# Kernel tuning notes

Measured on AMD Instinct MI355X. Metric: run time of the kernel, lower is better.

The kernel has to match this reference:

```python
import jax, jax.numpy as jnp
import numpy as np
from jax import lax

N, D, H = 8192, 256, 128
EPS = 1e-5


def _layernorm(x, g, b):
    m = jnp.mean(x, axis=-1, keepdims=True)
    v = jnp.mean((x - m) ** 2, axis=-1, keepdims=True)
    return (x - m) * jax.lax.rsqrt(v + EPS) * g + b


def setup_inputs() -> dict:
    key = jax.random.key(0)
    ks = jax.random.split(key, 8)
    s = 1.0 / np.sqrt(D)
    return {
        "x": jax.random.normal(ks[0], (N, D), jnp.float32),
        "wq": jax.random.normal(ks[1], (D, D), jnp.float32) * s,
        "bq": jnp.zeros((D,), jnp.float32),
        "wk": jax.random.normal(ks[2], (D, D), jnp.float32) * s,
        "bk": jnp.zeros((D,), jnp.float32),
        "wv": jax.random.normal(ks[3], (D, D), jnp.float32) * s,
        "bv": jnp.zeros((D,), jnp.float32),
        "cw": jax.random.normal(ks[4], (1, 1, 3, 3), jnp.float32) / 3.0,
        "cb": jnp.zeros((1,), jnp.float32),
        "m1w": jax.random.normal(ks[5], (H, D), jnp.float32) * s,
        "m2w": jax.random.normal(ks[6], (D, H), jnp.float32) / np.sqrt(H),
        "bng": jnp.ones((H,), jnp.float32),
        "bnb": jnp.zeros((H,), jnp.float32),
        "ln1g": jnp.ones((D,), jnp.float32),
        "ln1b": jnp.zeros((D,), jnp.float32),
        "ln2g": jnp.ones((D,), jnp.float32),
        "ln2b": jnp.zeros((D,), jnp.float32),
    }


def reference(x, wq, bq, wk, bk, wv, bv, cw, cb, m1w, m2w, bng, bnb, ln1g, ln1b, ln2g, ln2b):
    q = x @ wq.T + bq            # [N, D]
    k = x @ wk.T + bk
    v = x @ wv.T + bv
    # global Frobenius-norm normalization (torch.norm(q, p=2) over whole tensor)
    q = q / jnp.linalg.norm(q)
    k = k / jnp.linalg.norm(k)
    A = q @ k.T                  # [N, N]
    # 3x3 conv2d, 1->1 channel, padding SAME
    A4 = A[None, None, :, :]
    A4 = lax.conv_general_dilated(A4, cw, window_strides=(1, 1), padding="SAME")
    A4 = A4 + cb[None, :, None, None]
    agg_A = A4[0, 0]             # [N, N]
    attn = agg_A @ v             # [N, D]
    h = x + _layernorm(attn, ln1g, ln1b)
    # MLP with BatchNorm1d (training-mode batch stats, biased var)
    z = _layernorm(h, ln2g, ln2b) @ m1w.T          # [N, H]
    mu = jnp.mean(z, axis=0)
    var = jnp.mean((z - mu) ** 2, axis=0)
    z = (z - mu) * jax.lax.rsqrt(var + EPS) * bng + bnb
    z = jax.nn.relu(z)
    out = h + z @ m2w.T
    return out
```

## Files before the change

### kernel.cpp

```cpp
#include <hip/hip_runtime.h>
#include <hip/hip_bf16.h>
#include <math.h>


#define N_ 8192
#define D_ 256
#define H_ 128
#define EPSF 1e-5f

typedef unsigned short ushort_t;
typedef unsigned int uint_t;
typedef __attribute__((ext_vector_type(8))) short bf16x8;
typedef __attribute__((ext_vector_type(4))) short bf16x4;
typedef __attribute__((ext_vector_type(4))) float f32x4;

static const size_t OFF_QB  = 0;
static const size_t OFF_KT  = 4195328;
static const size_t OFF_VT  = 8389632;
static const size_t OFF_GP  = 12588032;
static const size_t OFF_MT  = 25170944;
static const size_t OFF_SVP = 25564160;
static const size_t OFF_SVC = 25826304;
static const size_t OFF_RED = 25827328;
static const size_t OFF_ZSP = 25829376;
static const size_t OFF_BNS = 26353664;
static const size_t OFF_WC  = 26354688;
static const size_t OFF_M1C = 26747904;
static const size_t OFF_M2C = 26813440;
static const size_t OFF_XB  = 26878976;
static const size_t WS_NEED = 31073280;

__device__ __forceinline__ ushort_t f2bf(float f) {
    __hip_bfloat16 h = __float2bfloat16(f);
    return reinterpret_cast<ushort_t&>(h);
}

__device__ __forceinline__ bf16x8 cvt8(float4 f0, float4 f1) {
    bf16x8 o;
    o[0] = (short)f2bf(f0.x); o[1] = (short)f2bf(f0.y);
    o[2] = (short)f2bf(f0.z); o[3] = (short)f2bf(f0.w);
    o[4] = (short)f2bf(f1.x); o[5] = (short)f2bf(f1.y);
    o[6] = (short)f2bf(f1.z); o[7] = (short)f2bf(f1.w);
    return o;
}

__device__ __forceinline__ float waveSum(float v)
{
#pragma unroll
    for (int o = 32; o > 0; o >>= 1) v += __shfl_xor(v, o);
    return v;
}

__global__ void prep_w(const float* __restrict__ wq, const float* __restrict__ wk,
                       const float* __restrict__ wv, const float* __restrict__ m1w,
                       const float* __restrict__ m2w, const float* __restrict__ x,
                       ushort_t* __restrict__ WC, ushort_t* __restrict__ M1C,
                       ushort_t* __restrict__ M2C, ushort_t* __restrict__ XB,
                       ushort_t* __restrict__ QbG, ushort_t* __restrict__ VTC)
{
    const int bid = blockIdx.x, tid = threadIdx.x;
    if (bid < 96) {
        const int sel = bid >> 5, kb = bid & 31;
        const float* W = (sel == 0) ? wq : ((sel == 1) ? wk : wv);
        const float* p = W + (size_t)tid * 256 + kb * 8;
        *(bf16x8*)(WC + (size_t)sel * 65536 + (size_t)kb * 2048 + (size_t)tid * 8)
            = cvt8(*(const float4*)p, *(const float4*)(p + 4));
    } else if (bid < 128) {
        const int kb = bid - 96;
        if (tid < 128) {
            const float* p = m1w + (size_t)tid * 256 + kb * 8;
            *(bf16x8*)(M1C + (size_t)kb * 1024 + (size_t)tid * 8)
                = cvt8(*(const float4*)p, *(const float4*)(p + 4));
        }
    } else if (bid < 144) {
        const int kb = bid - 128;
        const float* p = m2w + (size_t)tid * 128 + kb * 8;
        *(bf16x8*)(M2C + (size_t)kb * 2048 + (size_t)tid * 8)
            = cvt8(*(const float4*)p, *(const float4*)(p + 4));
    } else if (bid == 144) {
        QbG[tid] = 0; QbG[(size_t)8193 * 256 + tid] = 0;
        VTC[(size_t)tid * 8] = 0;
        VTC[((size_t)1024 * 256 + tid) * 8 + 1] = 0;
    } else {
        const size_t lin = (size_t)(bid - 145) * 2048 + (size_t)tid * 8;
        const float* p = x + lin;
        *(bf16x8*)(XB + lin) = cvt8(*(const float4*)p, *(const float4*)(p + 4));
    }
}

__global__ void __launch_bounds__(256)
qkv_mfma(const ushort_t* __restrict__ XB, const ushort_t* __restrict__ WC,
         const float* __restrict__ bq, const float* __restrict__ bk,
         const float* __restrict__ bv,
         ushort_t* __restrict__ QbG, ushort_t* __restrict__ KTC,
         ushort_t* __restrict__ VTC,
         float* __restrict__ RED, float* __restrict__ SVP)
{
    __shared__ ushort_t XS[32][264];
    __shared__ float lds4[4];
    const int tid = threadIdx.x, lane = tid & 63, wid = tid >> 6;
    const int sel = blockIdx.y;
    const int i0 = blockIdx.x * 32;
    const int jw = wid * 64;
    const int l15 = lane & 15, kg = lane >> 4;
    const ushort_t* Wc = WC + (size_t)sel * 65536;
    const float* B = (sel == 0) ? bq : ((sel == 1) ? bk : bv);

#pragma unroll
    for (int p = 0; p < 4; ++p) {
        int lin = p * 256 + tid;
        int row = lin >> 5;
        int c8  = (lin & 31) * 8;
        *(bf16x8*)(&XS[row][c8]) = *(const bf16x8*)(XB + (size_t)(i0 + row) * 256 + c8);
    }
    __syncthreads();

    f32x4 acc[2][4];
#pragma unroll
    for (int mi = 0; mi < 2; ++mi)
#pragma unroll
        for (int ni = 0; ni < 4; ++ni) acc[mi][ni] = 0.0f;

    for (int k0 = 0; k0 < 256; k0 += 32) {
        bf16x8 a[2], b[4];
#pragma unroll
        for (int mi = 0; mi < 2; ++mi)
            a[mi] = *(const bf16x8*)(&XS[16 * mi + l15][k0 + 8 * kg]);
#pragma unroll
        for (int ni = 0; ni < 4; ++ni)
            b[ni] = *(const bf16x8*)(Wc + (size_t)((k0 >> 3) + kg) * 2048
                                        + (size_t)(jw + 16 * ni + l15) * 8);
#pragma unroll
        for (int mi = 0; mi < 2; ++mi)
#pragma unroll
            for (int ni = 0; ni < 4; ++ni)
                acc[mi][ni] = __builtin_amdgcn_mfma_f32_16x16x32_bf16(a[mi], b[ni], acc[mi][ni], 0, 0, 0);
    }

    float ssq = 0.0f;
    float colp[4] = {0.0f, 0.0f, 0.0f, 0.0f};

    if (sel == 0) {
#pragma unroll
        for (int mi = 0; mi < 2; ++mi)
#pragma unroll
            for (int ni = 0; ni < 4; ++ni) {
                const int col = jw + 16 * ni + l15;
                const float bias = B[col];
#pragma unroll
                for (int r = 0; r < 4; ++r) {
                    const int row = i0 + 16 * mi + 4 * kg + r;
                    float val = acc[mi][ni][r] + bias;
                    QbG[(size_t)(row + 1) * 256 + col] = f2bf(val);
                    ssq = fmaf(val, val, ssq);
                }
            }
    } else if (sel == 1) {
#pragma unroll
        for (int mi = 0; mi < 2; ++mi)
#pragma unroll
            for (int ni = 0; ni < 4; ++ni) {
                const int col = jw + 16 * ni + l15;
                const float bias = B[col];
                const int tb = i0 + 16 * mi + 4 * kg;
                bf16x4 pk;
#pragma unroll
                for (int r = 0; r < 4; ++r) {
                    float val = acc[mi][ni][r] + bias;
                    ssq = fmaf(val, val, ssq);
                    pk[r] = (short)f2bf(val);
                }
                *(bf16x4*)(KTC + ((size_t)(tb >> 3) * 256 + col) * 8 + (tb & 7)) = pk;
            }
    } else {
#pragma unroll
        for (int mi = 0; mi < 2; ++mi)
#pragma unroll
            for (int ni = 0; ni < 4; ++ni) {
                const int col = jw + 16 * ni + l15;
                const float bias = B[col];
                const int tb = i0 + 16 * mi + 4 * kg;
                const int cb = tb >> 3, e0 = (tb & 7) + 1;
                float v0 = acc[mi][ni][0] + bias, v1 = acc[mi][ni][1] + bias;
                float v2 = acc[mi][ni][2] + bias, v3 = acc[mi][ni][3] + bias;
                colp[ni] += v0 + v1 + v2 + v3;
                ushort_t* p = VTC + ((size_t)cb * 256 + col) * 8 + e0;
                p[0] = f2bf(v0);
                *(uint_t*)(p + 1) = (uint_t)f2bf(v1) | ((uint_t)f2bf(v2) << 16);
                ushort_t v3b = f2bf(v3);
                if (e0 == 5)
                    VTC[((size_t)(cb + 1) * 256 + col) * 8] = v3b;
                else
                    p[3] = v3b;
            }
    }

    if (sel < 2) {
        float s = ssq;
#pragma unroll
        for (int o = 32; o > 0; o >>= 1) s += __shfl_down(s, o);
        if (lane == 0) lds4[wid] = s;
        __syncthreads();
        if (tid == 0)
            RED[sel * 256 + blockIdx.x] = lds4[0] + lds4[1] + lds4[2] + lds4[3];
    } else {
#pragma unroll
        for (int ni = 0; ni < 4; ++ni) {
            float v = colp[ni];
            v += __shfl_xor(v, 16);
            v += __shfl_xor(v, 32);
            if (kg == 0)
                SVP[(size_t)blockIdx.x * 256 + jw + 16 * ni + l15] = v;
        }
    }
}

__global__ void __launch_bounds__(256)
g_mfma(const ushort_t* __restrict__ KTC, const ushort_t* __restrict__ VTC,
       float* __restrict__ GP)
{
    const int tid = threadIdx.x, lane = tid & 63, wid = tid >> 6;
    const int d0 = blockIdx.x * 64 + (wid >> 1) * 32;
    const int jw = blockIdx.y * 32 + (wid & 1) * 16;
    const int ks = blockIdx.z;
    const int l15 = lane & 15, kg = lane >> 4;

    f32x4 acc[3][2];
#pragma unroll
    for (int v = 0; v < 3; ++v) { acc[v][0] = 0.0f; acc[v][1] = 0.0f; }

    for (int tt = 0; tt < 512; tt += 32) {
        const int t0 = ks * 512 + tt;
        const int cb0 = (t0 >> 3) + kg;
        bf16x8 a[2];
#pragma unroll
        for (int mi = 0; mi < 2; ++mi)
            a[mi] = *(const bf16x8*)(KTC + ((size_t)cb0 * 256 + (d0 + 16 * mi + l15)) * 8);

        const int j = jw + l15;
        uint4 r0 = *(const uint4*)(VTC + ((size_t)cb0 * 256 + j) * 8);
        uint_t rx = *(const uint_t*)(VTC + ((size_t)(cb0 + 1) * 256 + j) * 8);
        uint4 r2;
        r2.x = r0.y; r2.y = r0.z; r2.z = r0.w; r2.w = rx;
        uint4 m1;
        m1.x = (r0.x >> 16) | (r2.x << 16);
        m1.y = (r0.y >> 16) | (r2.y << 16);
        m1.z = (r0.z >> 16) | (r2.z << 16);
        m1.w = (r0.w >> 16) | (r2.w << 16);
        bf16x8 b2 = __builtin_bit_cast(bf16x8, r0);
        bf16x8 b0 = __builtin_bit_cast(bf16x8, r2);
        bf16x8 b1 = __builtin_bit_cast(bf16x8, m1);
#pragma unroll
        for (int mi = 0; mi < 2; ++mi) {
            acc[0][mi] = __builtin_amdgcn_mfma_f32_16x16x32_bf16(a[mi], b0, acc[0][mi], 0, 0, 0);
            acc[1][mi] = __builtin_amdgcn_mfma_f32_16x16x32_bf16(a[mi], b1, acc[1][mi], 0, 0, 0);
            acc[2][mi] = __builtin_amdgcn_mfma_f32_16x16x32_bf16(a[mi], b2, acc[2][mi], 0, 0, 0);
        }
    }

#pragma unroll
    for (int v = 0; v < 3; ++v) {
        float* gp = GP + (size_t)(ks * 3 + v) * 65536;
#pragma unroll
        for (int mi = 0; mi < 2; ++mi)
#pragma unroll
            for (int r = 0; r < 4; ++r)
                gp[(size_t)(d0 + 16 * mi + 4 * kg + r) * 256 + (jw + l15)]
                    = acc[v][mi][r];
    }
}

__global__ void combine_m(const float* __restrict__ GP, const float* __restrict__ cw,
                          const float* __restrict__ RED, const float* __restrict__ SVP,
                          const float* __restrict__ cb,
                          ushort_t* __restrict__ MTc, float* __restrict__ SVC)
{
    __shared__ float lds8[8];
    __shared__ float scsh;
    const int d = blockIdx.x, j = threadIdx.x;

    float sq = RED[j], sk = RED[256 + j];
#pragma unroll
    for (int o = 32; o > 0; o >>= 1) { sq += __shfl_down(sq, o); sk += __shfl_down(sk, o); }
    if ((j & 63) == 0) { lds8[j >> 6] = sq; lds8[4 + (j >> 6)] = sk; }

    float g[3] = {0.0f, 0.0f, 0.0f};
    for (int ks = 0; ks < 16; ++ks)
#pragma unroll
        for (int v = 0; v < 3; ++v)
            g[v] += GP[(size_t)(ks * 3 + v) * 65536 + (size_t)d * 256 + j];

    __syncthreads();
    if (j == 0) {
        float SQ = lds8[0] + lds8[1] + lds8[2] + lds8[3];
        float SK = lds8[4] + lds8[5] + lds8[6] + lds8[7];
        scsh = rsqrtf(SQ) * rsqrtf(SK);
    }
    __syncthreads();
    const float sc = scsh;

#pragma unroll
    for (int u = 0; u < 3; ++u) {
        float m = sc * (cw[u * 3 + 0] * g[0] + cw[u * 3 + 1] * g[1] + cw[u * 3 + 2] * g[2]);
        MTc[(size_t)u * 65536 + (size_t)(d >> 3) * 2048 + (size_t)j * 8 + (d & 7)]
            = f2bf(m);
    }
    if (d == 0) {
        float s = 0.0f;
        for (int b = 0; b < 256; ++b) s += SVP[(size_t)b * 256 + j];
        SVC[j] = cb[0] * s;
    }
}

__global__ void __launch_bounds__(512)
attn_ln_z_mfma(const ushort_t* __restrict__ QbG, const ushort_t* __restrict__ MTc,
               const float* __restrict__ SVC, const float* __restrict__ x,
               const float* __restrict__ ln1g, const float* __restrict__ ln1b,
               const float* __restrict__ ln2g, const float* __restrict__ ln2b,
               const ushort_t* __restrict__ M1C,
               float* __restrict__ h, float* __restrict__ Z,
               float* __restrict__ ZSP)
{
    __shared__ ushort_t QS[18][264];
    __shared__ float OUT[16][260];
    const int tid = threadIdx.x, lane = tid & 63, wid = tid >> 6;
    const int i0 = blockIdx.x * 16;
    const int jw = wid * 32;
    const int l15 = lane & 15, kg = lane >> 4;

    float4 xpre0 = *(const float4*)(x + (size_t)(i0 + wid * 2 + 0) * 256 + lane * 4);
    float4 xpre1 = *(const float4*)(x + (size_t)(i0 + wid * 2 + 1) * 256 + lane * 4);

    {
        int row = tid >> 5, c8 = (tid & 31) * 8;
        *(bf16x8*)(&QS[row][c8]) = *(const bf16x8*)(QbG + (size_t)(i0 + row) * 256 + c8);
        int idx = tid + 512;
        if (idx < 576) {
            row = idx >> 5; c8 = (idx & 31) * 8;
            *(bf16x8*)(&QS[row][c8]) = *(const bf16x8*)(QbG + (size_t)(i0 + row) * 256 + c8);
        }
    }
    __syncthreads();

    f32x4 acc[2];
    acc[0] = 0.0f; acc[1] = 0.0f;

    for (int k0 = 0; k0 < 256; k0 += 32) {
        bf16x8 a[3], b[3][2];
#pragma unroll
        for (int u = 0; u < 3; ++u)
            a[u] = *(const bf16x8*)(&QS[l15 + u][k0 + 8 * kg]);
#pragma unroll
        for (int u = 0; u < 3; ++u)
#pragma unroll
            for (int ni = 0; ni < 2; ++ni)
                b[u][ni] = *(const bf16x8*)(MTc + (size_t)u * 65536
                    + (size_t)((k0 >> 3) + kg) * 2048
                    + (size_t)(jw + 16 * ni + l15) * 8);
#pragma unroll
        for (int ni = 0; ni < 2; ++ni)
#pragma unroll
            for (int u = 0; u < 3; ++u)
                acc[ni] = __builtin_amdgcn_mfma_f32_16x16x32_bf16(
                    a[u], b[u][ni], acc[ni], 0, 0, 0);
    }

#pragma unroll
    for (int ni = 0; ni < 2; ++ni) {
        const int col = jw + 16 * ni + l15;
        const float sv = SVC[col];
#pragma unroll
        for (int r = 0; r < 4; ++r)
            OUT[4 * kg + r][col] = acc[ni][r] + sv;
    }
    __syncthreads();

    const float4 g14 = *(const float4*)(ln1g + lane * 4);
    const float4 b14 = *(const float4*)(ln1b + lane * 4);
    const float4 g24 = *(const float4*)(ln2g + lane * 4);
    const float4 b24 = *(const float4*)(ln2b + lane * 4);
#pragma unroll
    for (int rr = 0; rr < 2; ++rr) {
        const int row_l = wid * 2 + rr;
        const size_t off = (size_t)(i0 + row_l) * 256 + lane * 4;

        float4 a4 = *(const float4*)&OUT[row_l][lane * 4];
        float m = waveSum(a4.x + a4.y + a4.z + a4.w) * (1.0f / D_);
        float4 d4 = make_float4(a4.x - m, a4.y - m, a4.z - m, a4.w - m);
        float var = waveSum(d4.x * d4.x + d4.y * d4.y + d4.z * d4.z + d4.w * d4.w) * (1.0f / D_);
        float rs = rsqrtf(var + EPSF);

        float4 x4 = (rr == 0) ? xpre0 : xpre1;
        float4 h4;
        h4.x = x4.x + d4.x * rs * g14.x + b14.x;
        h4.y = x4.y + d4.y * rs * g14.y + b14.y;
        h4.z = x4.z + d4.z * rs * g14.z + b14.z;
        h4.w = x4.w + d4.w * rs * g14.w + b14.w;
        *(float4*)(h + off) = h4;

        float m2 = waveSum(h4.x + h4.y + h4.z + h4.w) * (1.0f / D_);
        float4 e4 = make_float4(h4.x - m2, h4.y - m2, h4.z - m2, h4.w - m2);
        float v2 = waveSum(e4.x * e4.x + e4.y * e4.y + e4.z * e4.z + e4.w * e4.w) * (1.0f / D_);
        float rs2 = rsqrtf(v2 + EPSF);

        float4 o4;
        o4.x = e4.x * rs2 * g24.x + b24.x;
        o4.y = e4.y * rs2 * g24.y + b24.y;
        o4.z = e4.z * rs2 * g24.z + b24.z;
        o4.w = e4.w * rs2 * g24.w + b24.w;
        *(float4*)&OUT[row_l][lane * 4] = o4;
    }
    __syncthreads();

    const int jz = wid * 16;
    f32x4 zacc;
    zacc = 0.0f;

    for (int k0 = 0; k0 < 256; k0 += 32) {
        bf16x8 a, b;
        {
            const float* lp = &OUT[l15][k0 + 8 * kg];
            a = cvt8(*(const float4*)lp, *(const float4*)(lp + 4));
        }
        b = *(const bf16x8*)(M1C + (size_t)((k0 >> 3) + kg) * 1024
                                  + (size_t)(jz + l15) * 8);
        zacc = __builtin_amdgcn_mfma_f32_16x16x32_bf16(a, b, zacc, 0, 0, 0);
    }

    float s = 0.0f, q = 0.0f;
    const int col = jz + l15;
#pragma unroll
    for (int r = 0; r < 4; ++r) {
        float zv = zacc[r];
        Z[(size_t)(i0 + 4 * kg + r) * 128 + col] = zv;
        s += zv;
        q = fmaf(zv, zv, q);
    }
    s += __shfl_xor(s, 16); s += __shfl_xor(s, 32);
    q += __shfl_xor(q, 16); q += __shfl_xor(q, 32);
    if (kg == 0) {
        ZSP[(size_t)blockIdx.x * 256 + col] = s;
        ZSP[(size_t)blockIdx.x * 256 + 128 + col] = q;
    }
}

__global__ void bn_reduce(const float* __restrict__ ZSP, float* __restrict__ BNS)
{
    __shared__ float red[8][32];
    const int tid = threadIdx.x;
    const int c0 = blockIdx.x * 32;
    const int cl = tid & 31, g = tid >> 5;
    float s = 0.0f;
    for (int b = g; b < 512; b += 8)
        s += ZSP[(size_t)b * 256 + c0 + cl];
    red[g][cl] = s;
    __syncthreads();
    if (tid < 32) {
        float t = 0.0f;
#pragma unroll
        for (int g2 = 0; g2 < 8; ++g2) t += red[g2][tid];
        BNS[c0 + tid] = t;
    }
}

__global__ void __launch_bounds__(512)
gemm_out_mfma(const float* __restrict__ Z, const ushort_t* __restrict__ M2C,
              const float* __restrict__ BNS,
              const float* __restrict__ bng, const float* __restrict__ bnb,
              float* __restrict__ out)
{
    __shared__ float bnA[128], bnB[128];
    __shared__ ushort_t XS[16][136];
    const int tid = threadIdx.x, lane = tid & 63, wid = tid >> 6;
    const int i0 = blockIdx.x * 16;
    const int jw = wid * 32;
    const int l15 = lane & 15, kg = lane >> 4;

    float oprev[2][4];
#pragma unroll
    for (int ni = 0; ni < 2; ++ni)
#pragma unroll
        for (int r = 0; r < 4; ++r)
            oprev[ni][r] = out[(size_t)(i0 + 4 * kg + r) * 256 + jw + 16 * ni + l15];

    if (tid < 128) {
        float s = BNS[tid], q = BNS[128 + tid];
        float mu = s * (1.0f / N_);
        float var = q * (1.0f / N_) - mu * mu;
        float aa = rsqrtf(var + EPSF) * bng[tid];
        bnA[tid] = aa;
        bnB[tid] = bnb[tid] - mu * aa;
    }
    __syncthreads();

    if (tid < 256) {
        int row = tid >> 4, c8 = (tid & 15) * 8;
        const float* zp = Z + (size_t)(i0 + row) * 128 + c8;
        float4 f0 = *(const float4*)zp;
        float4 f1 = *(const float4*)(zp + 4);
        float4 g0, g1;
        g0.x = fmaxf(fmaf(f0.x, bnA[c8 + 0], bnB[c8 + 0]), 0.0f);
        g0.y = fmaxf(fmaf(f0.y, bnA[c8 + 1], bnB[c8 + 1]), 0.0f);
        g0.z = fmaxf(fmaf(f0.z, bnA[c8 + 2], bnB[c8 + 2]), 0.0f);
        g0.w = fmaxf(fmaf(f0.w, bnA[c8 + 3], bnB[c8 + 3]), 0.0f);
        g1.x = fmaxf(fmaf(f1.x, bnA[c8 + 4], bnB[c8 + 4]), 0.0f);
        g1.y = fmaxf(fmaf(f1.y, bnA[c8 + 5], bnB[c8 + 5]), 0.0f);
        g1.z = fmaxf(fmaf(f1.z, bnA[c8 + 6], bnB[c8 + 6]), 0.0f);
        g1.w = fmaxf(fmaf(f1.w, bnA[c8 + 7], bnB[c8 + 7]), 0.0f);
        *(bf16x8*)(&XS[row][c8]) = cvt8(g0, g1);
    }
    __syncthreads();

    f32x4 acc[2];
    acc[0] = 0.0f; acc[1] = 0.0f;

    for (int k0 = 0; k0 < 128; k0 += 32) {
        bf16x8 a = *(const bf16x8*)(&XS[l15][k0 + 8 * kg]);
        bf16x8 b[2];
#pragma unroll
        for (int ni = 0; ni < 2; ++ni)
            b[ni] = *(const bf16x8*)(M2C + (size_t)((k0 >> 3) + kg) * 2048
                                          + (size_t)(jw + 16 * ni + l15) * 8);
#pragma unroll
        for (int ni = 0; ni < 2; ++ni)
            acc[ni] = __builtin_amdgcn_mfma_f32_16x16x32_bf16(a, b[ni], acc[ni], 0, 0, 0);
    }

#pragma unroll
    for (int ni = 0; ni < 2; ++ni)
#pragma unroll
        for (int r = 0; r < 4; ++r) {
            const size_t idx = (size_t)(i0 + 4 * kg + r) * 256
                             + (jw + 16 * ni + l15);
            out[idx] = oprev[ni][r] + acc[ni][r];
        }
}

extern "C" void kernel_launch(void* const* d_in, const int* in_sizes, int n_in,
                              void* d_out, int out_size, void* d_ws, size_t ws_size,
                              hipStream_t stream)
{
    const float* x    = (const float*)d_in[0];
    const float* wq   = (const float*)d_in[1];
    const float* bq   = (const float*)d_in[2];
    const float* wk   = (const float*)d_in[3];
    const float* bk   = (const float*)d_in[4];
    const float* wv   = (const float*)d_in[5];
    const float* bv   = (const float*)d_in[6];
    const float* cw   = (const float*)d_in[7];
    const float* cb   = (const float*)d_in[8];
    const float* m1w  = (const float*)d_in[9];
    const float* m2w  = (const float*)d_in[10];
    const float* bng  = (const float*)d_in[11];
    const float* bnb  = (const float*)d_in[12];
    const float* ln1g = (const float*)d_in[13];
    const float* ln1b = (const float*)d_in[14];
    const float* ln2g = (const float*)d_in[15];
    const float* ln2b = (const float*)d_in[16];

    float* outF = (float*)d_out;
    char*  wsb  = (char*)d_ws;
    if (ws_size < WS_NEED) return;

    ushort_t* QbG = (ushort_t*)(wsb + OFF_QB);
    ushort_t* KTC = (ushort_t*)(wsb + OFF_KT);
    ushort_t* VTC = (ushort_t*)(wsb + OFF_VT);
    float*    GP  = (float*)(wsb + OFF_GP);
    ushort_t* MTc = (ushort_t*)(wsb + OFF_MT);
    float*    SVP = (float*)(wsb + OFF_SVP);
    float*    SVC = (float*)(wsb + OFF_SVC);
    float*    RED = (float*)(wsb + OFF_RED);
    float*    ZSP = (float*)(wsb + OFF_ZSP);
    float*    BNS = (float*)(wsb + OFF_BNS);
    ushort_t* WC  = (ushort_t*)(wsb + OFF_WC);
    ushort_t* M1C = (ushort_t*)(wsb + OFF_M1C);
    ushort_t* M2C = (ushort_t*)(wsb + OFF_M2C);
    ushort_t* XB  = (ushort_t*)(wsb + OFF_XB);
    float*    Z   = (float*)(wsb + OFF_GP);

    const dim3 b256(256);
    const dim3 b512(512);

    prep_w<<<1169, b256, 0, stream>>>(wq, wk, wv, m1w, m2w, x,
                                      WC, M1C, M2C, XB, QbG, VTC);
    qkv_mfma<<<dim3(256, 3), b256, 0, stream>>>(XB, WC, bq, bk, bv,
                                                QbG, KTC, VTC, RED, SVP);
    g_mfma<<<dim3(4, 8, 16), b256, 0, stream>>>(KTC, VTC, GP);
    combine_m<<<256, b256, 0, stream>>>(GP, cw, RED, SVP, cb, MTc, SVC);
    attn_ln_z_mfma<<<512, b512, 0, stream>>>(QbG, MTc, SVC, x,
                                             ln1g, ln1b, ln2g, ln2b, M1C,
                                             outF, Z, ZSP);
    bn_reduce<<<8, b256, 0, stream>>>(ZSP, BNS);
    gemm_out_mfma<<<512, b512, 0, stream>>>(Z, M2C, BNS, bng, bnb, outF);
}
```

Measured before the change: 82.08 us.

## Fuse BN column reduction into attention kernel and retile g_mfma split-K

The separate bn_reduce launch is removed. Each attn_ln_z block now bumps a global counter after a threadfence, and the last block to finish sums the per-block ZSP partials into BNS, which saves one kernel launch. Separately, g_mfma is retiled to 32-row d tiles with 8 K-splits of 1024 instead of 16 splits of 512, which halves the partial GP buffers that combine_m must read. In exchange, the final reduction runs serially in a single block, and each g_mfma wave does less MFMA work per load, with longer K loops.

```diff
diff --git a/kernel.cpp b/kernel.cpp
--- a/kernel.cpp
+++ b/kernel.cpp
@@ -28,7 +28,8 @@
 static const size_t OFF_M1C = 26747904;
 static const size_t OFF_M2C = 26813440;
 static const size_t OFF_XB  = 26878976;
-static const size_t WS_NEED = 31073280;
+static const size_t OFF_CNT = 31073280;
+static const size_t WS_NEED = 31073344;
 
 __device__ __forceinline__ ushort_t f2bf(float f) {
     __hip_bfloat16 h = __float2bfloat16(f);
@@ -56,7 +57,8 @@
                        const float* __restrict__ m2w, const float* __restrict__ x,
                        ushort_t* __restrict__ WC, ushort_t* __restrict__ M1C,
                        ushort_t* __restrict__ M2C, ushort_t* __restrict__ XB,
-                       ushort_t* __restrict__ QbG, ushort_t* __restrict__ VTC)
+                       ushort_t* __restrict__ QbG, ushort_t* __restrict__ VTC,
+                       int* __restrict__ CNT)
 {
     const int bid = blockIdx.x, tid = threadIdx.x;
     if (bid < 96) {
@@ -81,6 +83,7 @@
         QbG[tid] = 0; QbG[(size_t)8193 * 256 + tid] = 0;
         VTC[(size_t)tid * 8] = 0;
         VTC[((size_t)1024 * 256 + tid) * 8 + 1] = 0;
+        if (tid == 0) CNT[0] = 0;
     } else {
         const size_t lin = (size_t)(bid - 145) * 2048 + (size_t)tid * 8;
         const float* p = x + lin;
@@ -220,22 +223,18 @@
        float* __restrict__ GP)
 {
     const int tid = threadIdx.x, lane = tid & 63, wid = tid >> 6;
-    const int d0 = blockIdx.x * 64 + (wid >> 1) * 32;
+    const int d0 = blockIdx.x * 32 + (wid >> 1) * 16;
     const int jw = blockIdx.y * 32 + (wid & 1) * 16;
     const int ks = blockIdx.z;
     const int l15 = lane & 15, kg = lane >> 4;
 
-    f32x4 acc[3][2];
-#pragma unroll
-    for (int v = 0; v < 3; ++v) { acc[v][0] = 0.0f; acc[v][1] = 0.0f; }
-
-    for (int tt = 0; tt < 512; tt += 32) {
-        const int t0 = ks * 512 + tt;
+    f32x4 acc[3];
+    acc[0] = 0.0f; acc[1] = 0.0f; acc[2] = 0.0f;
+
+    for (int tt = 0; tt < 1024; tt += 32) {
+        const int t0 = ks * 1024 + tt;
         const int cb0 = (t0 >> 3) + kg;
-        bf16x8 a[2];
-#pragma unroll
-        for (int mi = 0; mi < 2; ++mi)
-            a[mi] = *(const bf16x8*)(KTC + ((size_t)cb0 * 256 + (d0 + 16 * mi + l15)) * 8);
+        bf16x8 a = *(const bf16x8*)(KTC + ((size_t)cb0 * 256 + (d0 + l15)) * 8);
 
         const int j = jw + l15;
         uint4 r0 = *(const uint4*)(VTC + ((size_t)cb0 * 256 + j) * 8);
@@ -247,26 +246,17 @@
         m1.y = (r0.y >> 16) | (r2.y << 16);
         m1.z = (r0.z >> 16) | (r2.z << 16);
         m1.w = (r0.w >> 16) | (r2.w << 16);
-        bf16x8 b2 = __builtin_bit_cast(bf16x8, r0);
-        bf16x8 b0 = __builtin_bit_cast(bf16x8, r2);
-        bf16x8 b1 = __builtin_bit_cast(bf16x8, m1);
-#pragma unroll
-        for (int mi = 0; mi < 2; ++mi) {
-            acc[0][mi] = __builtin_amdgcn_mfma_f32_16x16x32_bf16(a[mi], b0, acc[0][mi], 0, 0, 0);
-            acc[1][mi] = __builtin_amdgcn_mfma_f32_16x16x32_bf16(a[mi], b1, acc[1][mi], 0, 0, 0);
-            acc[2][mi] = __builtin_amdgcn_mfma_f32_16x16x32_bf16(a[mi], b2, acc[2][mi], 0, 0, 0);
-        }
+        acc[0] = __builtin_amdgcn_mfma_f32_16x16x32_bf16(a, __builtin_bit_cast(bf16x8, r2), acc[0], 0, 0, 0);
+        acc[1] = __builtin_amdgcn_mfma_f32_16x16x32_bf16(a, __builtin_bit_cast(bf16x8, m1), acc[1], 0, 0, 0);
+        acc[2] = __builtin_amdgcn_mfma_f32_16x16x32_bf16(a, __builtin_bit_cast(bf16x8, r0), acc[2], 0, 0, 0);
     }
 
 #pragma unroll
     for (int v = 0; v < 3; ++v) {
         float* gp = GP + (size_t)(ks * 3 + v) * 65536;
 #pragma unroll
-        for (int mi = 0; mi < 2; ++mi)
-#pragma unroll
-            for (int r = 0; r < 4; ++r)
-                gp[(size_t)(d0 + 16 * mi + 4 * kg + r) * 256 + (jw + l15)]
-                    = acc[v][mi][r];
+        for (int r = 0; r < 4; ++r)
+            gp[(size_t)(d0 + 4 * kg + r) * 256 + (jw + l15)] = acc[v][r];
     }
 }
 
@@ -285,7 +275,7 @@
     if ((j & 63) == 0) { lds8[j >> 6] = sq; lds8[4 + (j >> 6)] = sk; }
 
     float g[3] = {0.0f, 0.0f, 0.0f};
-    for (int ks = 0; ks < 16; ++ks)
+    for (int ks = 0; ks < 8; ++ks)
 #pragma unroll
         for (int v = 0; v < 3; ++v)
             g[v] += GP[(size_t)(ks * 3 + v) * 65536 + (size_t)d * 256 + j];
@@ -319,10 +309,13 @@
                const float* __restrict__ ln2g, const float* __restrict__ ln2b,
                const ushort_t* __restrict__ M1C,
                float* __restrict__ h, float* __restrict__ Z,
-               float* __restrict__ ZSP)
+               float* __restrict__ ZSP, float* __restrict__ BNS,
+               int* __restrict__ CNT)
 {
     __shared__ ushort_t QS[18][264];
     __shared__ float OUT[16][260];
+    __shared__ int lastf;
+    __shared__ float pS[2][256];
     const int tid = threadIdx.x, lane = tid & 63, wid = tid >> 6;
     const int i0 = blockIdx.x * 16;
     const int jw = wid * 32;
@@ -442,24 +435,24 @@
         ZSP[(size_t)blockIdx.x * 256 + col] = s;
         ZSP[(size_t)blockIdx.x * 256 + 128 + col] = q;
     }
-}
-
-__global__ void bn_reduce(const float* __restrict__ ZSP, float* __restrict__ BNS)
-{
-    __shared__ float red[8][32];
-    const int tid = threadIdx.x;
-    const int c0 = blockIdx.x * 32;
-    const int cl = tid & 31, g = tid >> 5;
-    float s = 0.0f;
-    for (int b = g; b < 512; b += 8)
-        s += ZSP[(size_t)b * 256 + c0 + cl];
-    red[g][cl] = s;
-    __syncthreads();
-    if (tid < 32) {
+
+    __threadfence();
+    __syncthreads();
+    if (tid == 0) {
+        int old = atomicAdd(CNT, 1);
+        lastf = (old == 511) ? 1 : 0;
+    }
+    __syncthreads();
+    if (lastf) {
+        __threadfence();
+        const int c = tid & 255;
+        const int half = tid >> 8;
         float t = 0.0f;
-#pragma unroll
-        for (int g2 = 0; g2 < 8; ++g2) t += red[g2][tid];
-        BNS[c0 + tid] = t;
+        for (int b = half * 256; b < half * 256 + 256; ++b)
+            t += ZSP[(size_t)b * 256 + c];
+        pS[half][c] = t;
+        __syncthreads();
+        if (tid < 256) BNS[tid] = pS[0][tid] + pS[1][tid];
     }
 }
 
@@ -576,20 +569,20 @@
     ushort_t* M1C = (ushort_t*)(wsb + OFF_M1C);
     ushort_t* M2C = (ushort_t*)(wsb + OFF_M2C);
     ushort_t* XB  = (ushort_t*)(wsb + OFF_XB);
+    int*      CNT = (int*)(wsb + OFF_CNT);
     float*    Z   = (float*)(wsb + OFF_GP);
 
     const dim3 b256(256);
     const dim3 b512(512);
 
     prep_w<<<1169, b256, 0, stream>>>(wq, wk, wv, m1w, m2w, x,
-                                      WC, M1C, M2C, XB, QbG, VTC);
+                                      WC, M1C, M2C, XB, QbG, VTC, CNT);
     qkv_mfma<<<dim3(256, 3), b256, 0, stream>>>(XB, WC, bq, bk, bv,
                                                 QbG, KTC, VTC, RED, SVP);
-    g_mfma<<<dim3(4, 8, 16), b256, 0, stream>>>(KTC, VTC, GP);
+    g_mfma<<<dim3(8, 8, 8), b256, 0, stream>>>(KTC, VTC, GP);
     combine_m<<<256, b256, 0, stream>>>(GP, cw, RED, SVP, cb, MTc, SVC);
     attn_ln_z_mfma<<<512, b512, 0, stream>>>(QbG, MTc, SVC, x,
                                              ln1g, ln1b, ln2g, ln2b, M1C,
-                                             outF, Z, ZSP);
-    bn_reduce<<<8, b256, 0, stream>>>(ZSP, BNS);
+                                             outF, Z, ZSP, BNS, CNT);
     gemm_out_mfma<<<512, b512, 0, stream>>>(Z, M2C, BNS, bng, bnb, outF);
 }
```

Measured after the change: 239.3 us. 2.92x slower.
